# Optimization experiments

Hardware: AMD Instinct MI355X
Metric: run time of the kernel (lower is better)

Reference implementation:

```python
import jax, jax.numpy as jnp
import numpy as np

EPS = 1e-7  # K.epsilon()
ROUTINGS = 3
NUM_CAPSULE = 32
DIM_CAPSULE = 64

def _squash(x, axis=-1):
    # NOTE: this repo's 'squash' is just L2-ish normalization: x / sqrt(||x||^2 + eps)
    s2 = jnp.sum(jnp.square(x), axis=axis, keepdims=True)
    return x / jnp.sqrt(s2 + EPS)

def setup_inputs() -> dict:
    key = jax.random.key(0)
    k1, k2 = jax.random.split(key)
    u_vecs = jax.random.normal(k1, (32, 1024, 256), dtype=jnp.float32)
    # shared-weight capsule kernel: (1, input_dim_capsule, num_capsule*dim_capsule)
    W = jax.random.normal(k2, (1, 256, NUM_CAPSULE * DIM_CAPSULE), dtype=jnp.float32) * 0.05
    return {"u_vecs": u_vecs, "W": W}

def reference(u_vecs, W):
    B, N, D = u_vecs.shape
    # conv1d with width-1 kernel == matmul over feature dim
    u_hat = jnp.einsum('bnd,dm->bnm', u_vecs, W[0])          # [B, N, NC*DC]
    u_hat = u_hat.reshape(B, N, NUM_CAPSULE, DIM_CAPSULE)
    u_hat = jnp.transpose(u_hat, (0, 2, 1, 3))               # [B, NC, N, DC]

    b = jnp.zeros((B, NUM_CAPSULE, N), dtype=u_hat.dtype)    # routing logits
    v = None
    for i in range(ROUTINGS):
        c = jax.nn.softmax(b, axis=-1)                       # over input capsules
        s = jnp.einsum('bij,bijd->bid', c, u_hat)            # weighted sum
        v = _squash(s)                                       # [B, NC, DC]
        if i < ROUTINGS - 1:
            b = b + jnp.einsum('bid,bijd->bij', v, u_hat)    # agreement update
    return v
```

## Files before the change

kernel.cpp:

```cpp
#include <hip/hip_runtime.h>
#include <math.h>


typedef short v8s __attribute__((ext_vector_type(8)));
typedef short v4s __attribute__((ext_vector_type(4)));
typedef float v4f __attribute__((ext_vector_type(4)));

__device__ __forceinline__ unsigned short f2bf(float x) {
    unsigned u = __float_as_uint(x);
    u = u + 0x7fffu + ((u >> 16) & 1u);
    return (unsigned short)(u >> 16);
}
__device__ __forceinline__ float bf2f(unsigned short h) {
    return __uint_as_float(((unsigned)h) << 16);
}

__global__ __launch_bounds__(256) void k_init(const float* __restrict__ U,
                                              const float* __restrict__ W,
                                              float* __restrict__ t0p,
                                              float* __restrict__ WT) {
    int bid = blockIdx.x, tid = threadIdx.x;
    if (bid < 512) {
        int b = bid >> 4, q = bid & 15;
        const float* Up = U + (((b << 10) + (q << 6)) << 8) + tid;
        float acc = 0.f;
        #pragma unroll 16
        for (int jl = 0; jl < 64; ++jl) acc += Up[jl << 8];
        t0p[(b << 12) + (q << 8) + tid] = acc * (1.0f / 1024.0f);
    } else {
        __shared__ float tile[64 * 65];
        int tix = bid - 512;
        int k0 = (tix >> 5) << 6, c0 = (tix & 31) << 6;
        int cc = tid & 63, g4 = tid >> 6;
        #pragma unroll
        for (int r = 0; r < 16; ++r) {
            int kk = (g4 << 4) + r;
            tile[kk * 65 + cc] = W[(k0 + kk) * 2048 + c0 + cc];
        }
        __syncthreads();
        int kk = tid & 63;
        #pragma unroll
        for (int r = 0; r < 16; ++r) {
            int c = (g4 << 4) + r;
            WT[(c0 + c) * 256 + k0 + kk] = tile[kk * 65 + c];
        }
    }
}

__global__ __launch_bounds__(256) void k_sv(const float* __restrict__ t0p,
                                            const float* __restrict__ tpart,
                                            const float* __restrict__ sefpart,
                                            const float* __restrict__ W,
                                            const float* __restrict__ WT,
                                            short* __restrict__ wbt_h,
                                            short* __restrict__ wbt_l,
                                            float* __restrict__ out,
                                            int mode, int writeOut) {
    __shared__ float t_lds[256];
    __shared__ float spart[256];
    __shared__ __align__(16) float v_lds[64];
    __shared__ __align__(16) v4f spartw[256];
    __shared__ float sefv_s;
    int bid = blockIdx.x, tid = threadIdx.x;
    int b = bid >> 5, iG = bid & 31;
    int bg = (b << 1) | (iG >> 4), il = iG & 15;

    float acc = 0.f;
    if (mode == 0) {
        const float* tb = t0p + (b << 12) + tid;
        #pragma unroll
        for (int q = 0; q < 16; ++q) acc += tb[q << 8];
        if (tid == 0) sefv_s = 1.0f;
    } else {
        const float* tb = tpart + (((bg << 4) + il) << 8) + tid;
        #pragma unroll
        for (int p = 0; p < 16; ++p) acc += tb[p << 18];
        if (tid == 0) {
            float s = 0.f;
            #pragma unroll
            for (int p = 0; p < 16; ++p) s += sefpart[(p << 10) + (bg << 4) + il];
            sefv_s = s;
        }
    }
    t_lds[tid] = acc;
    __syncthreads();

    int d = tid & 63, kq = tid >> 6;
    const float* Wc = W + ((kq << 6) * 2048) + (iG << 6) + d;
    float s = 0.f;
    #pragma unroll 4
    for (int kk = 0; kk < 64; ++kk)
        s += t_lds[(kq << 6) + kk] * Wc[kk * 2048];
    spart[tid] = s;
    __syncthreads();

    if (tid < 64) {
        float sv = spart[tid] + spart[tid + 64] + spart[tid + 128] + spart[tid + 192];
        float n2 = sv * sv;
        #pragma unroll
        for (int m = 1; m < 64; m <<= 1) n2 += __shfl_xor(n2, m, 64);
        float sf = sefv_s;
        float v = sv * rsqrtf(n2 + 1e-7f * sf * sf);
        v_lds[tid] = v;
        if (writeOut) out[(bid << 6) + tid] = v;
    }
    __syncthreads();
    if (writeOut) return;

    int k4 = tid & 63, dq = tid >> 6;
    const float4* WT4 = (const float4*)WT;
    v4f wp = {0.f, 0.f, 0.f, 0.f};
    #pragma unroll
    for (int dd = 0; dd < 16; ++dd) {
        float vv = v_lds[(dq << 4) + dd];
        float4 wt = WT4[((iG << 6) + (dq << 4) + dd) * 64 + k4];
        wp.x += vv * wt.x; wp.y += vv * wt.y; wp.z += vv * wt.z; wp.w += vv * wt.w;
    }
    spartw[(dq << 6) + k4] = wp;
    __syncthreads();
    if (tid < 64) {
        v4f w = spartw[tid] + spartw[64 + tid] + spartw[128 + tid] + spartw[192 + tid];
        float wv4[4] = {w.x, w.y, w.z, w.w};
        unsigned short wh[4], wl[4];
        #pragma unroll
        for (int e = 0; e < 4; ++e) {
            wh[e] = f2bf(wv4[e]);
            wl[e] = f2bf(wv4[e] - bf2f(wh[e]));
        }
        int base = (((bg << 4) + il) << 8) + (tid << 2);
        *(v4s*)&wbt_h[base] = (v4s){(short)wh[0], (short)wh[1], (short)wh[2], (short)wh[3]};
        *(v4s*)&wbt_l[base] = (v4s){(short)wl[0], (short)wl[1], (short)wl[2], (short)wl[3]};
    }
}

__global__ __launch_bounds__(1024, 8) void k_pass(const float* __restrict__ U,
                                                  const short* __restrict__ wbt_h,
                                                  const short* __restrict__ wbt_l,
                                                  float* __restrict__ bmatg,
                                                  float* __restrict__ tpart_out,
                                                  float* __restrict__ sefpart_out,
                                                  int addold) {
    __shared__ short s_U[64 * 268];
    __shared__ short s_wh[16 * 264];
    __shared__ short s_wl[16 * 264];
    __shared__ short s_eh[16 * 72];
    __shared__ short s_el[16 * 72];
    __shared__ float s_red[16 * 320];
    __shared__ float s_sefp[16 * 16];

    const int tid = threadIdx.x, wv = tid >> 6, lane = tid & 63;
    const int quad = lane >> 4, nn = lane & 15;
    const int blk = blockIdx.x;
    const int b = blk & 31, pg = blk >> 5;
    const int p = pg >> 1, g2 = pg & 1;
    const int bg = (b << 1) | g2;
    const int rowbase = (b << 10) + (p << 6);
    const float4* U4 = (const float4*)U;

    const int mt2 = wv & 3, jq = wv >> 2;
    const int rr = (jq << 2) + quad;
    const int jloc = (mt2 << 4) + rr;
    const int ga = (((bg << 10) + (p << 6) + jloc) << 4) + nn;
    float bold = 0.f;
    if (addold) bold = bmatg[ga];

    if (tid < 512) {
        int row = tid >> 5, seg = tid & 31;
        int gidx = (((bg << 4) + row) << 8) + (seg << 3);
        *(v8s*)&s_wh[row * 264 + (seg << 3)] = *(const v8s*)(wbt_h + gidx);
        *(v8s*)&s_wl[row * 264 + (seg << 3)] = *(const v8s*)(wbt_l + gidx);
    }
    {
        int col = tid & 63, row0 = tid >> 6;
        float4 g[4];
        #pragma unroll
        for (int q = 0; q < 4; ++q)
            g[q] = U4[(rowbase + row0 + (q << 4)) * 64 + col];
        #pragma unroll
        for (int q = 0; q < 4; ++q)
            *(v4s*)&s_U[(row0 + (q << 4)) * 268 + (col << 2)] =
                (v4s){(short)f2bf(g[q].x), (short)f2bf(g[q].y),
                      (short)f2bf(g[q].z), (short)f2bf(g[q].w)};
    }
    __syncthreads();

    {
        const int mt = wv & 3, kq = wv >> 2;
        v4f dacc = {0.f, 0.f, 0.f, 0.f};
        #pragma unroll
        for (int c = 0; c < 2; ++c) {
            int kb = (kq << 6) + (c << 5) + (quad << 3);
            v8s a  = *(const v8s*)&s_U[((mt << 4) + nn) * 268 + kb];
            v8s bh = *(const v8s*)&s_wh[nn * 264 + kb];
            v8s bl = *(const v8s*)&s_wl[nn * 264 + kb];
            dacc = __builtin_amdgcn_mfma_f32_16x16x32_bf16(a, bh, dacc, 0, 0, 0);
            dacc = __builtin_amdgcn_mfma_f32_16x16x32_bf16(a, bl, dacc, 0, 0, 0);
        }
        #pragma unroll
        for (int r = 0; r < 4; ++r)
            s_red[wv * 320 + ((quad << 2) + r) * 20 + nn] = dacc[r];
    }
    __syncthreads();

    {
        float val = bold;
        #pragma unroll
        for (int kq = 0; kq < 4; ++kq)
            val += s_red[((kq << 2) + mt2) * 320 + rr * 20 + nn];
        if (!addold) bmatg[ga] = val;
        float e = __expf(val);
        unsigned short eh = f2bf(e);
        s_eh[nn * 72 + jloc] = (short)eh;
        s_el[nn * 72 + jloc] = (short)f2bf(e - bf2f(eh));
        float se = e;
        se += __shfl_xor(se, 16, 64);
        se += __shfl_xor(se, 32, 64);
        if (lane < 16) s_sefp[(wv << 4) + lane] = se;
    }
    __syncthreads();

    {
        v4f tacc = {0.f, 0.f, 0.f, 0.f};
        const int k0 = wv << 4;
        #pragma unroll
        for (int jc = 0; jc < 2; ++jc) {
            v8s aeh = *(const v8s*)&s_eh[nn * 72 + (jc << 5) + (quad << 3)];
            v8s ael = *(const v8s*)&s_el[nn * 72 + (jc << 5) + (quad << 3)];
            short bu[8];
            #pragma unroll
            for (int jj = 0; jj < 8; ++jj)
                bu[jj] = s_U[((jc << 5) + (quad << 3) + jj) * 268 + k0 + nn];
            v8s bf = (v8s){bu[0], bu[1], bu[2], bu[3], bu[4], bu[5], bu[6], bu[7]};
            tacc = __builtin_amdgcn_mfma_f32_16x16x32_bf16(aeh, bf, tacc, 0, 0, 0);
            tacc = __builtin_amdgcn_mfma_f32_16x16x32_bf16(ael, bf, tacc, 0, 0, 0);
        }
        #pragma unroll
        for (int r = 0; r < 4; ++r) {
            int i = (quad << 2) + r;
            tpart_out[(((((p << 6) + bg) << 4) + i) << 8) + k0 + nn] = tacc[r];
        }
    }
    if (tid < 16) {
        float ss = 0.f;
        #pragma unroll
        for (int w = 0; w < 16; ++w) ss += s_sefp[(w << 4) + tid];
        sefpart_out[(p << 10) + (bg << 4) + tid] = ss;
    }
}

extern "C" void kernel_launch(void* const* d_in, const int* in_sizes, int n_in,
                              void* d_out, int out_size, void* d_ws, size_t ws_size,
                              hipStream_t stream) {
    const float* U = (const float*)d_in[0];
    const float* W = (const float*)d_in[1];
    float* out = (float*)d_out;
    float* ws = (float*)d_ws;

    float* t0p   = ws;
    float* WT    = t0p + 131072;
    float* bmatg = WT + 524288;
    float* tp    = bmatg + 1048576;
    float* sef   = tp + 4194304;
    short* wbt_h = (short*)(sef + 16384);
    short* wbt_l = wbt_h + 262144;

    k_init<<<640, 256, 0, stream>>>(U, W, t0p, WT);
    k_sv<<<1024, 256, 0, stream>>>(t0p, nullptr, nullptr, W, WT,
                                   wbt_h, wbt_l, out, 0, 0);
    k_pass<<<1024, 1024, 0, stream>>>(U, wbt_h, wbt_l, bmatg, tp, sef, 0);
    k_sv<<<1024, 256, 0, stream>>>(t0p, tp, sef, W, WT,
                                   wbt_h, wbt_l, out, 1, 0);
    k_pass<<<1024, 1024, 0, stream>>>(U, wbt_h, wbt_l, bmatg, tp, sef, 1);
    k_sv<<<1024, 256, 0, stream>>>(t0p, tp, sef, W, WT,
                                   wbt_h, wbt_l, out, 1, 1);
}
```

Measured before the change: 131.0 us.

## Fuse routing passes into one persistent kernel with per-batch grid barriers

Merges the separate sv and pass kernels into one persistent kernel. Each block keeps its 64-row bf16 U tile resident in LDS across all routing iterations and handles both capsule groups for its batch. Blocks of the same batch synchronise through atomic-counter barriers, and partial sums are combined with global atomic adds instead of separate reduction buffers. Routing logits stay in registers rather than a global bmatg array, and the initial mean is computed while loading U. This removes repeated U reloads and several launches, but risks deadlock if the blocks of a batch are not co-resident, and atomic contention or spin waits could cost time.

Result: slower. 464.5 us (+254.5%).

```diff
diff --git a/kernel.cpp b/kernel.cpp
--- a/kernel.cpp
+++ b/kernel.cpp
@@ -14,23 +14,45 @@
 __device__ __forceinline__ float bf2f(unsigned short h) {
     return __uint_as_float(((unsigned)h) << 16);
 }
-
-__global__ __launch_bounds__(256) void k_init(const float* __restrict__ U,
-                                              const float* __restrict__ W,
-                                              float* __restrict__ t0p,
-                                              float* __restrict__ WT) {
+__device__ __forceinline__ float ald(const float* p) {
+    return __hip_atomic_load(p, __ATOMIC_RELAXED, __HIP_MEMORY_SCOPE_AGENT);
+}
+__device__ __forceinline__ void ast(float* p, float v) {
+    __hip_atomic_store(p, v, __ATOMIC_RELAXED, __HIP_MEMORY_SCOPE_AGENT);
+}
+__device__ __forceinline__ unsigned long long ald64(const void* p) {
+    return __hip_atomic_load((const unsigned long long*)p,
+                             __ATOMIC_RELAXED, __HIP_MEMORY_SCOPE_AGENT);
+}
+__device__ __forceinline__ void ast64(void* p, unsigned long long v) {
+    __hip_atomic_store((unsigned long long*)p, v,
+                       __ATOMIC_RELAXED, __HIP_MEMORY_SCOPE_AGENT);
+}
+
+__device__ __forceinline__ void bar_b(int* ctr, int b, int phase, int tid) {
+    __syncthreads();
+    if (tid == 0) {
+        __threadfence();
+        int* c = ctr + (b << 3) + phase;
+        __hip_atomic_fetch_add(c, 1, __ATOMIC_ACQ_REL,
+                               __HIP_MEMORY_SCOPE_AGENT);
+        while (__hip_atomic_load(c, __ATOMIC_ACQUIRE,
+                                 __HIP_MEMORY_SCOPE_AGENT) < 16)
+            __builtin_amdgcn_s_sleep(2);
+        __threadfence();
+    }
+    __syncthreads();
+}
+
+__global__ __launch_bounds__(256) void k_init(const float* __restrict__ W,
+                                              float* __restrict__ WT,
+                                              float* __restrict__ t,
+                                              float* __restrict__ sef,
+                                              int* __restrict__ ctr) {
     int bid = blockIdx.x, tid = threadIdx.x;
-    if (bid < 512) {
-        int b = bid >> 4, q = bid & 15;
-        const float* Up = U + (((b << 10) + (q << 6)) << 8) + tid;
-        float acc = 0.f;
-        #pragma unroll 16
-        for (int jl = 0; jl < 64; ++jl) acc += Up[jl << 8];
-        t0p[(b << 12) + (q << 8) + tid] = acc * (1.0f / 1024.0f);
-    } else {
+    if (bid < 128) {
         __shared__ float tile[64 * 65];
-        int tix = bid - 512;
-        int k0 = (tix >> 5) << 6, c0 = (tix & 31) << 6;
+        int k0 = (bid >> 5) << 6, c0 = (bid & 31) << 6;
         int cc = tid & 63, g4 = tid >> 6;
         #pragma unroll
         for (int r = 0; r < 16; ++r) {
@@ -44,208 +66,273 @@
             int c = (g4 << 4) + r;
             WT[(c0 + c) * 256 + k0 + kk] = tile[kk * 65 + c];
         }
-    }
-}
-
-__global__ __launch_bounds__(256) void k_sv(const float* __restrict__ t0p,
-                                            const float* __restrict__ tpart,
-                                            const float* __restrict__ sefpart,
-                                            const float* __restrict__ W,
-                                            const float* __restrict__ WT,
-                                            short* __restrict__ wbt_h,
-                                            short* __restrict__ wbt_l,
-                                            float* __restrict__ out,
-                                            int mode, int writeOut) {
-    __shared__ float t_lds[256];
-    __shared__ float spart[256];
-    __shared__ __align__(16) float v_lds[64];
-    __shared__ __align__(16) v4f spartw[256];
-    __shared__ float sefv_s;
-    int bid = blockIdx.x, tid = threadIdx.x;
-    int b = bid >> 5, iG = bid & 31;
-    int bg = (b << 1) | (iG >> 4), il = iG & 15;
-
-    float acc = 0.f;
-    if (mode == 0) {
-        const float* tb = t0p + (b << 12) + tid;
+    } else {
+        int z = bid - 128;
         #pragma unroll
-        for (int q = 0; q < 16; ++q) acc += tb[q << 8];
-        if (tid == 0) sefv_s = 1.0f;
-    } else {
-        const float* tb = tpart + (((bg << 4) + il) << 8) + tid;
-        #pragma unroll
-        for (int p = 0; p < 16; ++p) acc += tb[p << 18];
-        if (tid == 0) {
-            float s = 0.f;
-            #pragma unroll
-            for (int p = 0; p < 16; ++p) s += sefpart[(p << 10) + (bg << 4) + il];
-            sefv_s = s;
-        }
-    }
-    t_lds[tid] = acc;
-    __syncthreads();
-
-    int d = tid & 63, kq = tid >> 6;
-    const float* Wc = W + ((kq << 6) * 2048) + (iG << 6) + d;
-    float s = 0.f;
-    #pragma unroll 4
-    for (int kk = 0; kk < 64; ++kk)
-        s += t_lds[(kq << 6) + kk] * Wc[kk * 2048];
-    spart[tid] = s;
-    __syncthreads();
-
-    if (tid < 64) {
-        float sv = spart[tid] + spart[tid + 64] + spart[tid + 128] + spart[tid + 192];
-        float n2 = sv * sv;
-        #pragma unroll
-        for (int m = 1; m < 64; m <<= 1) n2 += __shfl_xor(n2, m, 64);
-        float sf = sefv_s;
-        float v = sv * rsqrtf(n2 + 1e-7f * sf * sf);
-        v_lds[tid] = v;
-        if (writeOut) out[(bid << 6) + tid] = v;
-    }
-    __syncthreads();
-    if (writeOut) return;
-
-    int k4 = tid & 63, dq = tid >> 6;
-    const float4* WT4 = (const float4*)WT;
-    v4f wp = {0.f, 0.f, 0.f, 0.f};
+        for (int r = 0; r < 16; ++r)
+            t[(z << 12) + (r << 8) + tid] = 0.f;
+        if (z == 0) {
+            #pragma unroll
+            for (int r = 0; r < 4; ++r) sef[(r << 8) + tid] = 0.f;
+            if (tid < 256) ctr[tid] = 0;
+        }
+    }
+}
+
+__device__ __forceinline__ void sv_block(
+    float* s_red, float* s_v, float* s_scal,
+    int b, int p, int tid, int wv, int lane,
+    const float* __restrict__ t0p, float* __restrict__ t,
+    float* __restrict__ sef, const float* __restrict__ W,
+    const float* __restrict__ WT, short* __restrict__ wbt_h,
+    short* __restrict__ wbt_l, float* __restrict__ out,
+    int mode, int final_out)
+{
     #pragma unroll
-    for (int dd = 0; dd < 16; ++dd) {
-        float vv = v_lds[(dq << 4) + dd];
-        float4 wt = WT4[((iG << 6) + (dq << 4) + dd) * 64 + k4];
-        wp.x += vv * wt.x; wp.y += vv * wt.y; wp.z += vv * wt.z; wp.w += vv * wt.w;
-    }
-    spartw[(dq << 6) + k4] = wp;
-    __syncthreads();
-    if (tid < 64) {
-        v4f w = spartw[tid] + spartw[64 + tid] + spartw[128 + tid] + spartw[192 + tid];
-        float wv4[4] = {w.x, w.y, w.z, w.w};
-        unsigned short wh[4], wl[4];
-        #pragma unroll
-        for (int e = 0; e < 4; ++e) {
-            wh[e] = f2bf(wv4[e]);
-            wl[e] = f2bf(wv4[e] - bf2f(wh[e]));
-        }
-        int base = (((bg << 4) + il) << 8) + (tid << 2);
-        *(v4s*)&wbt_h[base] = (v4s){(short)wh[0], (short)wh[1], (short)wh[2], (short)wh[3]};
-        *(v4s*)&wbt_l[base] = (v4s){(short)wl[0], (short)wl[1], (short)wl[2], (short)wl[3]};
-    }
-}
-
-__global__ __launch_bounds__(1024, 8) void k_pass(const float* __restrict__ U,
-                                                  const short* __restrict__ wbt_h,
-                                                  const short* __restrict__ wbt_l,
-                                                  float* __restrict__ bmatg,
-                                                  float* __restrict__ tpart_out,
-                                                  float* __restrict__ sefpart_out,
-                                                  int addold) {
+    for (int g2 = 0; g2 < 2; ++g2) {
+        const int iG = (g2 << 4) + p;
+        const int bg = (b << 1) | g2;
+        if (mode == 0) {
+            if (tid < 256) {
+                float a = 0.f;
+                #pragma unroll
+                for (int q = 0; q < 16; ++q)
+                    a += ald(&t0p[(b << 12) + (q << 8) + tid]);
+                s_red[tid] = a;
+            }
+            if (tid == 0) s_scal[0] = 1.0f;
+        } else {
+            if (tid < 256) {
+                const int o = (((bg << 4) + p) << 8) + tid;
+                s_red[tid] = ald(&t[o]);
+                if (!final_out) ast(&t[o], 0.f);
+            }
+            if (tid == 0) {
+                s_scal[0] = ald(&sef[(bg << 4) + p]);
+                if (!final_out) ast(&sef[(bg << 4) + p], 0.f);
+            }
+        }
+        __syncthreads();
+        {
+            const float* Wc = W + (iG << 6) + lane;
+            float sp = 0.f;
+            #pragma unroll
+            for (int kk = 0; kk < 16; ++kk) {
+                int k = (wv << 4) + kk;
+                sp += s_red[k] * Wc[k * 2048];
+            }
+            s_red[256 + (wv << 6) + lane] = sp;
+        }
+        __syncthreads();
+        if (tid < 64) {
+            float sv = 0.f;
+            #pragma unroll
+            for (int q = 0; q < 16; ++q) sv += s_red[256 + (q << 6) + tid];
+            float n2 = sv * sv;
+            #pragma unroll
+            for (int m = 1; m < 64; m <<= 1) n2 += __shfl_xor(n2, m, 64);
+            float sf = s_scal[0];
+            float vv = sv * rsqrtf(n2 + 1e-7f * sf * sf);
+            if (final_out) out[(b << 11) + (iG << 6) + tid] = vv;
+            else s_v[tid] = vv;
+        }
+        __syncthreads();
+        if (final_out) continue;
+        {
+            const float4* WT4 = (const float4*)WT;
+            v4f wp = {0.f, 0.f, 0.f, 0.f};
+            #pragma unroll
+            for (int e = 0; e < 4; ++e) {
+                int d = (wv << 2) + e;
+                float vd = s_v[d];
+                float4 wt = WT4[(((iG << 6) + d) << 6) + lane];
+                wp.x += vd * wt.x; wp.y += vd * wt.y;
+                wp.z += vd * wt.z; wp.w += vd * wt.w;
+            }
+            ((v4f*)s_red)[(wv << 6) + lane] = wp;
+        }
+        __syncthreads();
+        if (tid < 64) {
+            v4f w = {0.f, 0.f, 0.f, 0.f};
+            #pragma unroll
+            for (int q = 0; q < 16; ++q) w += ((v4f*)s_red)[(q << 6) + tid];
+            float wv4[4] = {w.x, w.y, w.z, w.w};
+            unsigned short wh[4], wl[4];
+            #pragma unroll
+            for (int e = 0; e < 4; ++e) {
+                wh[e] = f2bf(wv4[e]);
+                wl[e] = f2bf(wv4[e] - bf2f(wh[e]));
+            }
+            union { v4s s; unsigned long long u; } ch, cl;
+            ch.s = (v4s){(short)wh[0], (short)wh[1], (short)wh[2], (short)wh[3]};
+            cl.s = (v4s){(short)wl[0], (short)wl[1], (short)wl[2], (short)wl[3]};
+            const int bsx = (((bg << 4) + p) << 8) + (tid << 2);
+            ast64(&wbt_h[bsx], ch.u);
+            ast64(&wbt_l[bsx], cl.u);
+        }
+        __syncthreads();
+    }
+}
+
+__device__ __forceinline__ void pass_block(
+    short* s_U, short* s_wh, short* s_wl, short* s_eh, short* s_el,
+    float* s_red, float* s_sefp,
+    int b, int tid, int wv, int lane, int quad, int nn,
+    const short* __restrict__ wbt_h, const short* __restrict__ wbt_l,
+    float* __restrict__ t, float* __restrict__ sef,
+    float* vlog, int pass)
+{
+    const int mt2 = wv & 3, jq = wv >> 2;
+    const int rr = (jq << 2) + quad;
+    const int jloc = (mt2 << 4) + rr;
+    #pragma unroll
+    for (int g2 = 0; g2 < 2; ++g2) {
+        const int bg = (b << 1) | g2;
+        if (tid < 512) {
+            int row = tid >> 5, seg = tid & 31;
+            int gidx = (((bg << 4) + row) << 8) + (seg << 3);
+            unsigned long long h0 = ald64(&wbt_h[gidx]);
+            unsigned long long h1 = ald64(&wbt_h[gidx + 4]);
+            unsigned long long l0 = ald64(&wbt_l[gidx]);
+            unsigned long long l1 = ald64(&wbt_l[gidx + 4]);
+            *(unsigned long long*)&s_wh[row * 264 + (seg << 3)]     = h0;
+            *(unsigned long long*)&s_wh[row * 264 + (seg << 3) + 4] = h1;
+            *(unsigned long long*)&s_wl[row * 264 + (seg << 3)]     = l0;
+            *(unsigned long long*)&s_wl[row * 264 + (seg << 3) + 4] = l1;
+        }
+        __syncthreads();
+        {
+            const int mt = wv & 3, kq = wv >> 2;
+            v4f dacc = {0.f, 0.f, 0.f, 0.f};
+            #pragma unroll
+            for (int c = 0; c < 2; ++c) {
+                int kb = (kq << 6) + (c << 5) + (quad << 3);
+                v8s a  = *(const v8s*)&s_U[((mt << 4) + nn) * 268 + kb];
+                v8s bh = *(const v8s*)&s_wh[nn * 264 + kb];
+                v8s bl = *(const v8s*)&s_wl[nn * 264 + kb];
+                dacc = __builtin_amdgcn_mfma_f32_16x16x32_bf16(a, bh, dacc, 0, 0, 0);
+                dacc = __builtin_amdgcn_mfma_f32_16x16x32_bf16(a, bl, dacc, 0, 0, 0);
+            }
+            #pragma unroll
+            for (int r = 0; r < 4; ++r)
+                s_red[wv * 320 + ((quad << 2) + r) * 20 + nn] = dacc[r];
+        }
+        __syncthreads();
+        {
+            float val = pass ? vlog[g2] : 0.f;
+            #pragma unroll
+            for (int kq = 0; kq < 4; ++kq)
+                val += s_red[((kq << 2) + mt2) * 320 + rr * 20 + nn];
+            if (!pass) vlog[g2] = val;
+            float e = __expf(val);
+            unsigned short eh = f2bf(e);
+            s_eh[nn * 72 + jloc] = (short)eh;
+            s_el[nn * 72 + jloc] = (short)f2bf(e - bf2f(eh));
+            float se = e;
+            se += __shfl_xor(se, 16, 64);
+            se += __shfl_xor(se, 32, 64);
+            if (lane < 16) s_sefp[(wv << 4) + lane] = se;
+        }
+        __syncthreads();
+        {
+            v4f tacc = {0.f, 0.f, 0.f, 0.f};
+            const int k0 = wv << 4;
+            #pragma unroll
+            for (int jc = 0; jc < 2; ++jc) {
+                v8s aeh = *(const v8s*)&s_eh[nn * 72 + (jc << 5) + (quad << 3)];
+                v8s ael = *(const v8s*)&s_el[nn * 72 + (jc << 5) + (quad << 3)];
+                short bu[8];
+                #pragma unroll
+                for (int jj = 0; jj < 8; ++jj)
+                    bu[jj] = s_U[((jc << 5) + (quad << 3) + jj) * 268 + k0 + nn];
+                v8s bf = (v8s){bu[0], bu[1], bu[2], bu[3],
+                               bu[4], bu[5], bu[6], bu[7]};
+                tacc = __builtin_amdgcn_mfma_f32_16x16x32_bf16(aeh, bf, tacc, 0, 0, 0);
+                tacc = __builtin_amdgcn_mfma_f32_16x16x32_bf16(ael, bf, tacc, 0, 0, 0);
+            }
+            #pragma unroll
+            for (int r = 0; r < 4; ++r) {
+                int i = (quad << 2) + r;
+                unsafeAtomicAdd(&t[(((bg << 4) + i) << 8) + k0 + nn], tacc[r]);
+            }
+        }
+        if (tid < 16) {
+            float ss = 0.f;
+            #pragma unroll
+            for (int w = 0; w < 16; ++w) ss += s_sefp[(w << 4) + tid];
+            unsafeAtomicAdd(&sef[(bg << 4) + tid], ss);
+        }
+        __syncthreads();
+    }
+}
+
+__global__ __launch_bounds__(1024, 8) void k_big(
+    const float* __restrict__ U, const float* __restrict__ W,
+    const float* __restrict__ WT, float* __restrict__ t0p,
+    float* __restrict__ t, float* __restrict__ sef,
+    short* __restrict__ wbt_h, short* __restrict__ wbt_l,
+    int* __restrict__ ctr, float* __restrict__ out)
+{
     __shared__ short s_U[64 * 268];
     __shared__ short s_wh[16 * 264];
     __shared__ short s_wl[16 * 264];
     __shared__ short s_eh[16 * 72];
     __shared__ short s_el[16 * 72];
-    __shared__ float s_red[16 * 320];
+    __shared__ __align__(16) float s_red[16 * 320];
     __shared__ float s_sefp[16 * 16];
+    __shared__ __align__(16) float s_v[64];
+    __shared__ float s_scal[2];
 
     const int tid = threadIdx.x, wv = tid >> 6, lane = tid & 63;
     const int quad = lane >> 4, nn = lane & 15;
     const int blk = blockIdx.x;
-    const int b = blk & 31, pg = blk >> 5;
-    const int p = pg >> 1, g2 = pg & 1;
-    const int bg = (b << 1) | g2;
+    const int b = blk >> 4, p = blk & 15;
     const int rowbase = (b << 10) + (p << 6);
-    const float4* U4 = (const float4*)U;
-
-    const int mt2 = wv & 3, jq = wv >> 2;
-    const int rr = (jq << 2) + quad;
-    const int jloc = (mt2 << 4) + rr;
-    const int ga = (((bg << 10) + (p << 6) + jloc) << 4) + nn;
-    float bold = 0.f;
-    if (addold) bold = bmatg[ga];
-
-    if (tid < 512) {
-        int row = tid >> 5, seg = tid & 31;
-        int gidx = (((bg << 4) + row) << 8) + (seg << 3);
-        *(v8s*)&s_wh[row * 264 + (seg << 3)] = *(const v8s*)(wbt_h + gidx);
-        *(v8s*)&s_wl[row * 264 + (seg << 3)] = *(const v8s*)(wbt_l + gidx);
-    }
+    float vlog[2];
+
     {
+        v4f* cp4 = (v4f*)s_red;
+        const float4* U4 = (const float4*)U;
         int col = tid & 63, row0 = tid >> 6;
-        float4 g[4];
+        v4f psum = {0.f, 0.f, 0.f, 0.f};
         #pragma unroll
-        for (int q = 0; q < 4; ++q)
-            g[q] = U4[(rowbase + row0 + (q << 4)) * 64 + col];
-        #pragma unroll
-        for (int q = 0; q < 4; ++q)
+        for (int q = 0; q < 4; ++q) {
+            float4 g = U4[(rowbase + row0 + (q << 4)) * 64 + col];
+            psum.x += g.x; psum.y += g.y; psum.z += g.z; psum.w += g.w;
             *(v4s*)&s_U[(row0 + (q << 4)) * 268 + (col << 2)] =
-                (v4s){(short)f2bf(g[q].x), (short)f2bf(g[q].y),
-                      (short)f2bf(g[q].z), (short)f2bf(g[q].w)};
-    }
-    __syncthreads();
-
-    {
-        const int mt = wv & 3, kq = wv >> 2;
-        v4f dacc = {0.f, 0.f, 0.f, 0.f};
-        #pragma unroll
-        for (int c = 0; c < 2; ++c) {
-            int kb = (kq << 6) + (c << 5) + (quad << 3);
-            v8s a  = *(const v8s*)&s_U[((mt << 4) + nn) * 268 + kb];
-            v8s bh = *(const v8s*)&s_wh[nn * 264 + kb];
-            v8s bl = *(const v8s*)&s_wl[nn * 264 + kb];
-            dacc = __builtin_amdgcn_mfma_f32_16x16x32_bf16(a, bh, dacc, 0, 0, 0);
-            dacc = __builtin_amdgcn_mfma_f32_16x16x32_bf16(a, bl, dacc, 0, 0, 0);
-        }
-        #pragma unroll
-        for (int r = 0; r < 4; ++r)
-            s_red[wv * 320 + ((quad << 2) + r) * 20 + nn] = dacc[r];
-    }
-    __syncthreads();
-
-    {
-        float val = bold;
-        #pragma unroll
-        for (int kq = 0; kq < 4; ++kq)
-            val += s_red[((kq << 2) + mt2) * 320 + rr * 20 + nn];
-        if (!addold) bmatg[ga] = val;
-        float e = __expf(val);
-        unsigned short eh = f2bf(e);
-        s_eh[nn * 72 + jloc] = (short)eh;
-        s_el[nn * 72 + jloc] = (short)f2bf(e - bf2f(eh));
-        float se = e;
-        se += __shfl_xor(se, 16, 64);
-        se += __shfl_xor(se, 32, 64);
-        if (lane < 16) s_sefp[(wv << 4) + lane] = se;
-    }
-    __syncthreads();
-
-    {
-        v4f tacc = {0.f, 0.f, 0.f, 0.f};
-        const int k0 = wv << 4;
-        #pragma unroll
-        for (int jc = 0; jc < 2; ++jc) {
-            v8s aeh = *(const v8s*)&s_eh[nn * 72 + (jc << 5) + (quad << 3)];
-            v8s ael = *(const v8s*)&s_el[nn * 72 + (jc << 5) + (quad << 3)];
-            short bu[8];
-            #pragma unroll
-            for (int jj = 0; jj < 8; ++jj)
-                bu[jj] = s_U[((jc << 5) + (quad << 3) + jj) * 268 + k0 + nn];
-            v8s bf = (v8s){bu[0], bu[1], bu[2], bu[3], bu[4], bu[5], bu[6], bu[7]};
-            tacc = __builtin_amdgcn_mfma_f32_16x16x32_bf16(aeh, bf, tacc, 0, 0, 0);
-            tacc = __builtin_amdgcn_mfma_f32_16x16x32_bf16(ael, bf, tacc, 0, 0, 0);
-        }
-        #pragma unroll
-        for (int r = 0; r < 4; ++r) {
-            int i = (quad << 2) + r;
-            tpart_out[(((((p << 6) + bg) << 4) + i) << 8) + k0 + nn] = tacc[r];
-        }
-    }
-    if (tid < 16) {
-        float ss = 0.f;
-        #pragma unroll
-        for (int w = 0; w < 16; ++w) ss += s_sefp[(w << 4) + tid];
-        sefpart_out[(p << 10) + (bg << 4) + tid] = ss;
-    }
+                (v4s){(short)f2bf(g.x), (short)f2bf(g.y),
+                      (short)f2bf(g.z), (short)f2bf(g.w)};
+        }
+        cp4[(row0 << 6) + col] = psum;
+        __syncthreads();
+        if (tid < 256) {
+            const float* cp = (const float*)cp4;
+            float acc = 0.f;
+            #pragma unroll
+            for (int r0 = 0; r0 < 16; ++r0) acc += cp[(r0 << 8) + tid];
+            ast(&t0p[(b << 12) + (p << 8) + tid], acc * (1.0f / 1024.0f));
+        }
+    }
+    bar_b(ctr, b, 0, tid);
+
+    sv_block(s_red, s_v, s_scal, b, p, tid, wv, lane,
+             t0p, t, sef, W, WT, wbt_h, wbt_l, out, 0, 0);
+    bar_b(ctr, b, 1, tid);
+
+    pass_block(s_U, s_wh, s_wl, s_eh, s_el, s_red, s_sefp,
+               b, tid, wv, lane, quad, nn, wbt_h, wbt_l, t, sef, vlog, 0);
+    bar_b(ctr, b, 2, tid);
+
+    sv_block(s_red, s_v, s_scal, b, p, tid, wv, lane,
+             t0p, t, sef, W, WT, wbt_h, wbt_l, out, 1, 0);
+    bar_b(ctr, b, 3, tid);
+
+    pass_block(s_U, s_wh, s_wl, s_eh, s_el, s_red, s_sefp,
+               b, tid, wv, lane, quad, nn, wbt_h, wbt_l, t, sef, vlog, 1);
+    bar_b(ctr, b, 4, tid);
+
+    sv_block(s_red, s_v, s_scal, b, p, tid, wv, lane,
+             t0p, t, sef, W, WT, wbt_h, wbt_l, out, 1, 1);
 }
 
 extern "C" void kernel_launch(void* const* d_in, const int* in_sizes, int n_in,
@@ -258,19 +345,13 @@
 
     float* t0p   = ws;
     float* WT    = t0p + 131072;
-    float* bmatg = WT + 524288;
-    float* tp    = bmatg + 1048576;
-    float* sef   = tp + 4194304;
-    short* wbt_h = (short*)(sef + 16384);
+    float* t     = WT + 524288;
+    float* sef   = t + 262144;
+    short* wbt_h = (short*)(sef + 1024);
     short* wbt_l = wbt_h + 262144;
-
-    k_init<<<640, 256, 0, stream>>>(U, W, t0p, WT);
-    k_sv<<<1024, 256, 0, stream>>>(t0p, nullptr, nullptr, W, WT,
-                                   wbt_h, wbt_l, out, 0, 0);
-    k_pass<<<1024, 1024, 0, stream>>>(U, wbt_h, wbt_l, bmatg, tp, sef, 0);
-    k_sv<<<1024, 256, 0, stream>>>(t0p, tp, sef, W, WT,
-                                   wbt_h, wbt_l, out, 1, 0);
-    k_pass<<<1024, 1024, 0, stream>>>(U, wbt_h, wbt_l, bmatg, tp, sef, 1);
-    k_sv<<<1024, 256, 0, stream>>>(t0p, tp, sef, W, WT,
-                                   wbt_h, wbt_l, out, 1, 1);
-}
+    int*   ctr   = (int*)(wbt_l + 262144);
+
+    k_init<<<192, 256, 0, stream>>>(W, WT, t, sef, ctr);
+    k_big<<<512, 1024, 0, stream>>>(U, W, WT, t0p, t, sef,
+                                    wbt_h, wbt_l, ctr, out);
+}
```

## Process both capsule groups per block in k_pass, reusing the staged U tile

Applied to the files above, without the earlier changes.

Each k_pass block now handles both capsule halves (g2=0,1) for a 64-row U tile, so the U tile is loaded and converted to bf16 once instead of twice and the grid halves to 512 blocks. The agreement GEMM drops the split-K across waves: 8 waves each compute a full-K dot product, which removes the s_red reduction buffer and one barrier. The weighted-sum stage has each wave do two output tiles. The cost is half the waves idling during the first MFMA phase, longer serial K loops, and fewer blocks to spread across the GPU.

After: 133.1 us. No clear change (+1.6%).

```diff
diff --git a/kernel.cpp b/kernel.cpp
--- a/kernel.cpp
+++ b/kernel.cpp
@@ -141,36 +141,20 @@
                                                   float* __restrict__ sefpart_out,
                                                   int addold) {
     __shared__ short s_U[64 * 268];
-    __shared__ short s_wh[16 * 264];
-    __shared__ short s_wl[16 * 264];
-    __shared__ short s_eh[16 * 72];
-    __shared__ short s_el[16 * 72];
-    __shared__ float s_red[16 * 320];
-    __shared__ float s_sefp[16 * 16];
+    __shared__ short s_wh[2 * 16 * 264];
+    __shared__ short s_wl[2 * 16 * 264];
+    __shared__ short s_eh[2 * 16 * 72];
+    __shared__ short s_el[2 * 16 * 72];
+    __shared__ float s_sefp[8 * 16];
 
     const int tid = threadIdx.x, wv = tid >> 6, lane = tid & 63;
     const int quad = lane >> 4, nn = lane & 15;
     const int blk = blockIdx.x;
-    const int b = blk & 31, pg = blk >> 5;
-    const int p = pg >> 1, g2 = pg & 1;
-    const int bg = (b << 1) | g2;
+    const int b = blk & 31, p = blk >> 5;
     const int rowbase = (b << 10) + (p << 6);
-    const float4* U4 = (const float4*)U;
-
-    const int mt2 = wv & 3, jq = wv >> 2;
-    const int rr = (jq << 2) + quad;
-    const int jloc = (mt2 << 4) + rr;
-    const int ga = (((bg << 10) + (p << 6) + jloc) << 4) + nn;
-    float bold = 0.f;
-    if (addold) bold = bmatg[ga];
-
-    if (tid < 512) {
-        int row = tid >> 5, seg = tid & 31;
-        int gidx = (((bg << 4) + row) << 8) + (seg << 3);
-        *(v8s*)&s_wh[row * 264 + (seg << 3)] = *(const v8s*)(wbt_h + gidx);
-        *(v8s*)&s_wl[row * 264 + (seg << 3)] = *(const v8s*)(wbt_l + gidx);
-    }
+
     {
+        const float4* U4 = (const float4*)U;
         int col = tid & 63, row0 = tid >> 6;
         float4 g[4];
         #pragma unroll
@@ -181,70 +165,80 @@
             *(v4s*)&s_U[(row0 + (q << 4)) * 268 + (col << 2)] =
                 (v4s){(short)f2bf(g[q].x), (short)f2bf(g[q].y),
                       (short)f2bf(g[q].z), (short)f2bf(g[q].w)};
-    }
-    __syncthreads();
-
-    {
-        const int mt = wv & 3, kq = wv >> 2;
+        int row = tid >> 5, seg = tid & 31;
+        int gidx = (((b << 5) + row) << 8) + (seg << 3);
+        int lidx = (row >> 4) * 4224 + (row & 15) * 264 + (seg << 3);
+        *(v8s*)&s_wh[lidx] = *(const v8s*)(wbt_h + gidx);
+        *(v8s*)&s_wl[lidx] = *(const v8s*)(wbt_l + gidx);
+    }
+    __syncthreads();
+
+    if (wv < 8) {
+        const int jt = wv & 3, g2 = wv >> 2;
+        const int bg = (b << 1) | g2;
         v4f dacc = {0.f, 0.f, 0.f, 0.f};
         #pragma unroll
-        for (int c = 0; c < 2; ++c) {
-            int kb = (kq << 6) + (c << 5) + (quad << 3);
-            v8s a  = *(const v8s*)&s_U[((mt << 4) + nn) * 268 + kb];
-            v8s bh = *(const v8s*)&s_wh[nn * 264 + kb];
-            v8s bl = *(const v8s*)&s_wl[nn * 264 + kb];
+        for (int c = 0; c < 8; ++c) {
+            int kb = (c << 5) + (quad << 3);
+            v8s a  = *(const v8s*)&s_U[((jt << 4) + nn) * 268 + kb];
+            v8s bh = *(const v8s*)&s_wh[g2 * 4224 + nn * 264 + kb];
+            v8s bl = *(const v8s*)&s_wl[g2 * 4224 + nn * 264 + kb];
             dacc = __builtin_amdgcn_mfma_f32_16x16x32_bf16(a, bh, dacc, 0, 0, 0);
             dacc = __builtin_amdgcn_mfma_f32_16x16x32_bf16(a, bl, dacc, 0, 0, 0);
         }
-        #pragma unroll
-        for (int r = 0; r < 4; ++r)
-            s_red[wv * 320 + ((quad << 2) + r) * 20 + nn] = dacc[r];
-    }
-    __syncthreads();
-
-    {
-        float val = bold;
-        #pragma unroll
-        for (int kq = 0; kq < 4; ++kq)
-            val += s_red[((kq << 2) + mt2) * 320 + rr * 20 + nn];
-        if (!addold) bmatg[ga] = val;
-        float e = __expf(val);
-        unsigned short eh = f2bf(e);
-        s_eh[nn * 72 + jloc] = (short)eh;
-        s_el[nn * 72 + jloc] = (short)f2bf(e - bf2f(eh));
-        float se = e;
+        float se = 0.f;
+        #pragma unroll
+        for (int r = 0; r < 4; ++r) {
+            int jloc = (jt << 4) + (quad << 2) + r;
+            int ga = (((bg << 10) + (p << 6) + jloc) << 4) + nn;
+            float val = dacc[r];
+            if (addold) val += bmatg[ga];
+            else bmatg[ga] = val;
+            float e = __expf(val);
+            unsigned short eh = f2bf(e);
+            s_eh[g2 * 1152 + nn * 72 + jloc] = (short)eh;
+            s_el[g2 * 1152 + nn * 72 + jloc] = (short)f2bf(e - bf2f(eh));
+            se += e;
+        }
         se += __shfl_xor(se, 16, 64);
         se += __shfl_xor(se, 32, 64);
-        if (lane < 16) s_sefp[(wv << 4) + lane] = se;
+        if (lane < 16) s_sefp[((g2 << 2) + jt) << 4 | lane] = se;
     }
     __syncthreads();
 
     {
-        v4f tacc = {0.f, 0.f, 0.f, 0.f};
-        const int k0 = wv << 4;
-        #pragma unroll
-        for (int jc = 0; jc < 2; ++jc) {
-            v8s aeh = *(const v8s*)&s_eh[nn * 72 + (jc << 5) + (quad << 3)];
-            v8s ael = *(const v8s*)&s_el[nn * 72 + (jc << 5) + (quad << 3)];
-            short bu[8];
+        const int g2 = wv >> 3, kt2 = wv & 7;
+        const int bg = (b << 1) | g2;
+        #pragma unroll
+        for (int task = 0; task < 2; ++task) {
+            const int k0 = ((task << 3) + kt2) << 4;
+            v4f tacc = {0.f, 0.f, 0.f, 0.f};
             #pragma unroll
-            for (int jj = 0; jj < 8; ++jj)
-                bu[jj] = s_U[((jc << 5) + (quad << 3) + jj) * 268 + k0 + nn];
-            v8s bf = (v8s){bu[0], bu[1], bu[2], bu[3], bu[4], bu[5], bu[6], bu[7]};
-            tacc = __builtin_amdgcn_mfma_f32_16x16x32_bf16(aeh, bf, tacc, 0, 0, 0);
-            tacc = __builtin_amdgcn_mfma_f32_16x16x32_bf16(ael, bf, tacc, 0, 0, 0);
-        }
-        #pragma unroll
-        for (int r = 0; r < 4; ++r) {
-            int i = (quad << 2) + r;
-            tpart_out[(((((p << 6) + bg) << 4) + i) << 8) + k0 + nn] = tacc[r];
-        }
-    }
-    if (tid < 16) {
+            for (int jc = 0; jc < 2; ++jc) {
+                v8s aeh = *(const v8s*)&s_eh[g2 * 1152 + nn * 72 + (jc << 5) + (quad << 3)];
+                v8s ael = *(const v8s*)&s_el[g2 * 1152 + nn * 72 + (jc << 5) + (quad << 3)];
+                short bu[8];
+                #pragma unroll
+                for (int jj = 0; jj < 8; ++jj)
+                    bu[jj] = s_U[((jc << 5) + (quad << 3) + jj) * 268 + k0 + nn];
+                v8s bf = (v8s){bu[0], bu[1], bu[2], bu[3],
+                               bu[4], bu[5], bu[6], bu[7]};
+                tacc = __builtin_amdgcn_mfma_f32_16x16x32_bf16(aeh, bf, tacc, 0, 0, 0);
+                tacc = __builtin_amdgcn_mfma_f32_16x16x32_bf16(ael, bf, tacc, 0, 0, 0);
+            }
+            #pragma unroll
+            for (int r = 0; r < 4; ++r) {
+                int i = (quad << 2) + r;
+                tpart_out[(((((p << 6) + bg) << 4) + i) << 8) + k0 + nn] = tacc[r];
+            }
+        }
+    }
+    if (tid < 32) {
+        int g2 = tid >> 4, i = tid & 15;
         float ss = 0.f;
         #pragma unroll
-        for (int w = 0; w < 16; ++w) ss += s_sefp[(w << 4) + tid];
-        sefpart_out[(p << 10) + (bg << 4) + tid] = ss;
+        for (int jt = 0; jt < 4; ++jt) ss += s_sefp[((g2 << 2) + jt) << 4 | i];
+        sefpart_out[(p << 10) + (((b << 1) | g2) << 4) + i] = ss;
     }
 }
 
@@ -260,17 +254,17 @@
     float* WT    = t0p + 131072;
     float* bmatg = WT + 524288;
     float* tp    = bmatg + 1048576;
-    float* sef   = tp + 4194304;
-    short* wbt_h = (short*)(sef + 16384);
+    float* sefp  = tp + 4194304;
+    short* wbt_h = (short*)(sefp + 16384);
     short* wbt_l = wbt_h + 262144;
 
     k_init<<<640, 256, 0, stream>>>(U, W, t0p, WT);
-    k_sv<<<1024, 256, 0, stream>>>(t0p, nullptr, nullptr, W, WT,
+    k_sv<<<1024, 256, 0, stream>>>(t0p, tp, sefp, W, WT,
                                    wbt_h, wbt_l, out, 0, 0);
-    k_pass<<<1024, 1024, 0, stream>>>(U, wbt_h, wbt_l, bmatg, tp, sef, 0);
-    k_sv<<<1024, 256, 0, stream>>>(t0p, tp, sef, W, WT,
+    k_pass<<<512, 1024, 0, stream>>>(U, wbt_h, wbt_l, bmatg, tp, sefp, 0);
+    k_sv<<<1024, 256, 0, stream>>>(t0p, tp, sefp, W, WT,
                                    wbt_h, wbt_l, out, 1, 0);
-    k_pass<<<1024, 1024, 0, stream>>>(U, wbt_h, wbt_l, bmatg, tp, sef, 1);
-    k_sv<<<1024, 256, 0, stream>>>(t0p, tp, sef, W, WT,
+    k_pass<<<512, 1024, 0, stream>>>(U, wbt_h, wbt_l, bmatg, tp, sefp, 1);
+    k_sv<<<1024, 256, 0, stream>>>(t0p, tp, sefp, W, WT,
                                    wbt_h, wbt_l, out, 1, 1);
 }
```
